# Kernel optimization log

Measured on AMD Instinct MI355X. Metric: run time of the kernel, lower is better.

Reference implementation:

```python
import jax, jax.numpy as jnp
from jax import lax
import numpy as np

SCALES = 3
DIR_PROFILE = [2, 3, 4]


def _gaussian_lowpass():
    ks, sigma = 5, 1.0
    ax = np.arange(-ks // 2 + 1.0, ks // 2 + 1.0)
    g = np.exp(-0.5 * np.square(ax) / sigma ** 2)
    k1 = g / g.sum()
    k2 = np.outer(k1, k1)
    k2 = k2 / k2.sum()
    return k2.astype(np.float32)  # [5, 5]


def _oriented_filter(angle, scale):
    size = 15
    sx, sy = 2.0 * scale, 0.5 * scale
    x = np.arange(-size // 2 + 1, size // 2 + 1)
    y = np.arange(-size // 2 + 1, size // 2 + 1)
    X, Y = np.meshgrid(x, y)
    Xr = X * np.cos(angle) - Y * np.sin(angle)
    Yr = X * np.sin(angle) + Y * np.cos(angle)
    k = np.exp(-0.5 * (Xr ** 2 / sx ** 2 + Yr ** 2 / sy ** 2)) * Xr / sx ** 2
    k = k - k.mean()
    n = np.linalg.norm(k)
    if n > 1e-6:
        k = k / n
    return k.astype(np.float32)  # [15, 15]


LP_FILTER = jnp.asarray(_gaussian_lowpass())[None, None]  # [1,1,5,5]
DIR_FILTERS = []  # per scale: [n_dirs, 1, 15, 15]
for _s, _lvl in enumerate(DIR_PROFILE):
    _nd = 2 ** _lvl
    _fs = np.stack([_oriented_filter(np.pi * d / _nd, _s + 1) for d in range(_nd)])
    DIR_FILTERS.append(jnp.asarray(_fs)[:, None])


def _depthwise(x, kernel):
    # x: [N, 1, H, W]; kernel: [O, 1, kh, kw]; reflect-pad 'same' cross-correlation
    kh, kw = kernel.shape[2], kernel.shape[3]
    xp = jnp.pad(x, ((0, 0), (0, 0), (kh // 2, kh // 2), (kw // 2, kw // 2)), mode='reflect')
    return lax.conv_general_dilated(xp, kernel, (1, 1), 'VALID',
                                    dimension_numbers=('NCHW', 'OIHW', 'NCHW'))


def setup_inputs() -> dict:
    key = jax.random.key(0)
    x = jax.random.normal(key, (8, 3, 384, 384), dtype=jnp.float32)
    return {"x": x}


def reference(x) -> jnp.ndarray:
    B, C, H, W = x.shape
    xc = x.reshape(B * C, 1, H, W)  # each RGB channel processed independently

    # Non-subsampled Laplacian pyramid: bandpasses + final lowpass
    bandpasses = []
    current = xc
    for _ in range(SCALES):
        lp = _depthwise(current, LP_FILTER)
        bandpasses.append(current - lp)
        current = lp

    # Directional filter bank per scale (all directions in one grouped conv)
    feats = []
    for s in range(SCALES):
        feats.append(_depthwise(bandpasses[s], DIR_FILTERS[s]))  # [B*C, 2^lvl, H, W]
    feats.append(current)  # final lowpass [B*C, 1, H, W]

    out = jnp.concatenate(feats, axis=1)  # [B*C, 29, H, W]
    return out.reshape(B, C * out.shape[1], H, W)  # [B, 87, H, W]
```

## Files before the change

kernel.cpp:

```cpp
#include <hip/hip_runtime.h>

#define HH 384
#define WW 384
#define HWSZ (HH * WW)
#define NIMG 24

#define SYM0 0
#define ASYM0 126
#define SYM1 238
#define ASYM1 490
#define SYM2 714
#define ASYM2 1218

__device__ __forceinline__ int refl(int i, int n) {
    if (i < 0) i = -i;
    if (i >= n) i = 2 * n - 2 - i;
    return i;
}

__device__ const float LPW[5] = {
    0.054488684549642945f, 0.24420134200323332f, 0.40261994689424746f,
    0.24420134200323332f, 0.054488684549642945f
};

__global__ __launch_bounds__(256) void gen_filters(double* __restrict__ gtmp) {
    int f = blockIdx.x;
    int s, d, nd;
    if (f < 4)       { s = 0; nd = 4;  d = f;      }
    else if (f < 12) { s = 1; nd = 8;  d = f - 4;  }
    else             { s = 2; nd = 16; d = f - 12; }

    double angle = M_PI * (double)d / (double)nd;
    double scale = (double)(s + 1);
    double sx = 2.0 * scale, sy = 0.5 * scale;

    int tid = threadIdx.x;
    double val = 0.0;
    if (tid < 225) {
        int row = tid / 15, col = tid % 15;
        double X = (double)(col - 7);
        double Y = (double)(row - 7);
        double ca = cos(angle), sa = sin(angle);
        double Xr = X * ca - Y * sa;
        double Yr = X * sa + Y * ca;
        val = exp(-0.5 * (Xr * Xr / (sx * sx) + Yr * Yr / (sy * sy))) * Xr / (sx * sx);
    }

    __shared__ double red[256];
    red[tid] = val;
    __syncthreads();
    for (int st = 128; st > 0; st >>= 1) {
        if (tid < st) red[tid] += red[tid + st];
        __syncthreads();
    }
    double mean = red[0] / 225.0;
    __syncthreads();

    double dv = (tid < 225) ? (val - mean) : 0.0;
    red[tid] = dv * dv;
    __syncthreads();
    for (int st = 128; st > 0; st >>= 1) {
        if (tid < st) red[tid] += red[tid + st];
        __syncthreads();
    }
    double nrm = sqrt(red[0]);
    double inv = (nrm > 1e-6) ? (1.0 / nrm) : 1.0;

    if (tid < 225) {
        gtmp[(long)f * 225 + tid] = (val - mean) * inv;
    }
}

__global__ __launch_bounds__(256) void pack_tables(
    const double* __restrict__ gtmp, float* __restrict__ tab) {
    int s = blockIdx.x;
    int nh = (s == 0) ? 2 : (s == 1) ? 4 : 8;
    int fbase = (s == 0) ? 0 : (s == 1) ? 4 : 12;
    int symoff = (s == 0) ? SYM0 : (s == 1) ? SYM1 : SYM2;
    int asymoff = (s == 0) ? ASYM0 : (s == 1) ? ASYM1 : ASYM2;
    int nsym = 63 * nh, nasym = 56 * nh;

    for (int t = threadIdx.x; t < nsym + nasym; t += 256) {
        bool issym = t < nsym;
        int tt = issym ? t : t - nsym;
        int j = tt / nh, k = tt % nh;
        int u, v;
        if (issym) {
            if (j < 7)       { u = 0;         v = j + 1; }
            else if (j < 14) { u = j - 6;     v = 0;     }
            else { int p = j - 14; u = p / 7 + 1; v = p % 7 + 1; }
        } else {
            if (j < 7)       { u = 0;         v = j + 1; }
            else { int p = j - 7; u = p / 7 + 1; v = p % 7 + 1; }
        }
        int d = (k == 0) ? (issym ? nh : 0) : k;
        const double* F = gtmp + (long)(fbase + d) * 225;
        double gp = F[(7 + u) * 15 + (7 + v)];
        double gm = F[(7 + u) * 15 + (7 - v)];
        double val = issym ? 0.5 * (gp + gm) : 0.5 * (gp - gm);
        tab[(issym ? symoff : asymoff) + j * nh + k] = (float)val;
    }
}

__global__ __launch_bounds__(256) void lp_kernel(
    const float* __restrict__ in, float* __restrict__ out, long ostride) {
    int n = blockIdx.z;
    int x = blockIdx.x * 32 + threadIdx.x;
    int y = blockIdx.y * 8 + threadIdx.y;
    const float* ip = in + (long)n * HWSZ;

    float acc = 0.f;
#pragma unroll
    for (int fy = 0; fy < 5; ++fy) {
        int yy = refl(y + fy - 2, HH);
        const float* rp = ip + yy * WW;
        float rs = 0.f;
#pragma unroll
        for (int fx = 0; fx < 5; ++fx) {
            int xx = refl(x + fx - 2, WW);
            rs = fmaf(LPW[fx], rp[xx], rs);
        }
        acc = fmaf(LPW[fy], rs, acc);
    }
    out[(long)n * ostride + y * WW + x] = acc;
}

template <int NH, int R>
__global__ __launch_bounds__(256, 4) void dir_kernel(
    const float* __restrict__ A, long as,
    const float* __restrict__ B, long bs,
    const float* __restrict__ symt, const float* __restrict__ asymt,
    float* __restrict__ out, int c0) {
    constexpr int TH = 8 * R;
    __shared__ float sm[TH + 14][48];

    int n = blockIdx.z;
    int tx = threadIdx.x, ty = threadIdx.y;
    int bx = blockIdx.x * 32, by = blockIdx.y * TH;

    const float* Ab = A + (long)n * as;
    const float* Bb = B + (long)n * bs;

    int lid = ty * 32 + tx;
    for (int l = lid; l < (TH + 14) * 46; l += 256) {
        int ly = l / 46, lx = l % 46;
        int gy = refl(by + ly - 7, HH);
        int gx = refl(bx + lx - 7, WW);
        long gi = (long)gy * WW + gx;
        sm[ly][lx] = Ab[gi] - Bb[gi];
    }
    __syncthreads();

    float accP[NH][R], accQ[NH][R];
#pragma unroll
    for (int k = 0; k < NH; ++k)
#pragma unroll
        for (int r = 0; r < R; ++r) { accP[k][r] = 0.f; accQ[k][r] = 0.f; }

    int xc = tx + 7;

#pragma unroll
    for (int v = 1; v <= 7; ++v) {
        float dv[R];
#pragma unroll
        for (int r = 0; r < R; ++r) {
            int yb = ty + 7 + 8 * r;
            dv[r] = sm[yb][xc + v] - sm[yb][xc - v];
        }
#pragma unroll
        for (int k = 0; k < NH; ++k) {
            float cs = symt[(v - 1) * NH + k];
            float ca = asymt[(v - 1) * NH + k];
#pragma unroll
            for (int r = 0; r < R; ++r) {
                accP[k][r] = fmaf(cs, dv[r], accP[k][r]);
                accQ[k][r] = fmaf(ca, dv[r], accQ[k][r]);
            }
        }
    }

#pragma unroll 1
    for (int u = 1; u <= 7; ++u) {
        {
            float dvc[R];
#pragma unroll
            for (int r = 0; r < R; ++r) {
                int yb = ty + 7 + 8 * r;
                dvc[r] = sm[yb + u][xc] - sm[yb - u][xc];
            }
#pragma unroll
            for (int k = 0; k < NH; ++k) {
                float cs = symt[(6 + u) * NH + k];
#pragma unroll
                for (int r = 0; r < R; ++r)
                    accP[k][r] = fmaf(cs, dvc[r], accP[k][r]);
            }
        }
#pragma unroll
        for (int v = 1; v <= 7; ++v) {
            float S[R], D[R];
#pragma unroll
            for (int r = 0; r < R; ++r) {
                int yb = ty + 7 + 8 * r;
                float a = sm[yb + u][xc + v];
                float b = sm[yb + u][xc - v];
                float c = sm[yb - u][xc + v];
                float d = sm[yb - u][xc - v];
                float t1 = a - d, t2 = b - c;
                S[r] = t1 + t2;
                D[r] = t1 - t2;
            }
            int jp = (u - 1) * 7 + (v - 1);
#pragma unroll
            for (int k = 0; k < NH; ++k) {
                float cs = symt[(14 + jp) * NH + k];
                float ca = asymt[(7 + jp) * NH + k];
#pragma unroll
                for (int r = 0; r < R; ++r) {
                    accP[k][r] = fmaf(cs, S[r], accP[k][r]);
                    accQ[k][r] = fmaf(ca, D[r], accQ[k][r]);
                }
            }
        }
    }

    long ob = ((long)n * 29 + c0) * HWSZ;
#pragma unroll
    for (int r = 0; r < R; ++r) {
        long idx = ob + (long)(by + ty + r * 8) * WW + bx + tx;
        out[idx] = accQ[0][r];
        out[idx + (long)NH * HWSZ] = accP[0][r];
#pragma unroll
        for (int k = 1; k < NH; ++k) {
            out[idx + (long)k * HWSZ] = accP[k][r] + accQ[k][r];
            out[idx + (long)(2 * NH - k) * HWSZ] = accP[k][r] - accQ[k][r];
        }
    }
}

extern "C" void kernel_launch(void* const* d_in, const int* in_sizes, int n_in,
                              void* d_out, int out_size, void* d_ws, size_t ws_size,
                              hipStream_t stream) {
    const float* x = (const float*)d_in[0];
    float* out = (float*)d_out;
    float* ws = (float*)d_ws;

    float* tab = ws;
    float* lp0 = ws + 2048;
    float* lp1 = lp0 + (long)NIMG * HWSZ;
    double* gtmp = (double*)lp0;

    gen_filters<<<28, 256, 0, stream>>>(gtmp);
    pack_tables<<<3, 256, 0, stream>>>(gtmp, tab);

    dim3 blk(32, 8);
    dim3 lpgrid(12, 48, NIMG);
    lp_kernel<<<lpgrid, blk, 0, stream>>>(x, lp0, HWSZ);
    lp_kernel<<<lpgrid, blk, 0, stream>>>(lp0, lp1, HWSZ);
    lp_kernel<<<lpgrid, blk, 0, stream>>>(lp1, out + 28l * HWSZ, 29l * HWSZ);

    dir_kernel<2, 4><<<dim3(12, 12, NIMG), blk, 0, stream>>>(
        x, HWSZ, lp0, HWSZ, tab + SYM0, tab + ASYM0, out, 0);
    dir_kernel<4, 4><<<dim3(12, 12, NIMG), blk, 0, stream>>>(
        lp0, HWSZ, lp1, HWSZ, tab + SYM1, tab + ASYM1, out, 4);
    dir_kernel<8, 2><<<dim3(12, 24, NIMG), blk, 0, stream>>>(
        lp1, HWSZ, out + 28l * HWSZ, 29l * HWSZ, tab + SYM2, tab + ASYM2, out, 12);
}
```

Before: 638.4 us.

## Fuse lowpass pyramid into one kernel and bake filter tables at compile time

The three separate lowpass launches become one tiled kernel that loads a haloed input tile into shared memory and runs the separable 5-tap filter three times in place, writing lp0, lp1 and the final lowpass. The two filter-generation and table-packing kernels are replaced by constexpr tables evaluated at compile time, so coefficients become immediates in the fully unrolled directional loop. The unrolled loop may raise register pressure or code size. The fused lowpass also recomputes halo rows and adds several block barriers.

```diff
diff --git a/kernel.cpp b/kernel.cpp
--- a/kernel.cpp
+++ b/kernel.cpp
@@ -5,13 +5,6 @@
 #define HWSZ (HH * WW)
 #define NIMG 24
 
-#define SYM0 0
-#define ASYM0 126
-#define SYM1 238
-#define ASYM1 490
-#define SYM2 714
-#define ASYM2 1218
-
 __device__ __forceinline__ int refl(int i, int n) {
     if (i < 0) i = -i;
     if (i >= n) i = 2 * n - 2 - i;
@@ -23,113 +16,206 @@
     0.24420134200323332f, 0.054488684549642945f
 };
 
-__global__ __launch_bounds__(256) void gen_filters(double* __restrict__ gtmp) {
-    int f = blockIdx.x;
-    int s, d, nd;
-    if (f < 4)       { s = 0; nd = 4;  d = f;      }
-    else if (f < 12) { s = 1; nd = 8;  d = f - 4;  }
-    else             { s = 2; nd = 16; d = f - 12; }
-
-    double angle = M_PI * (double)d / (double)nd;
+constexpr double CPI = 3.141592653589793;
+
+constexpr double cexp(double x) {
+    int k = 0; double t = x;
+    while (t > 0.25 || t < -0.25) { t *= 0.5; ++k; }
+    double sum = 1.0, term = 1.0;
+    for (int n = 1; n <= 14; ++n) { term *= t / n; sum += term; }
+    for (int i = 0; i < k; ++i) sum *= sum;
+    return sum;
+}
+constexpr double ccos(double x) {
+    double sgn = 1.0;
+    if (x > CPI * 0.5) { x = CPI - x; sgn = -1.0; }
+    double x2 = x * x, sum = 1.0, term = 1.0;
+    for (int n = 1; n <= 12; ++n) { term *= -x2 / ((2.0 * n - 1) * (2.0 * n)); sum += term; }
+    return sgn * sum;
+}
+constexpr double csin(double x) {
+    if (x > CPI * 0.5) x = CPI - x;
+    double x2 = x * x, sum = x, term = x;
+    for (int n = 1; n <= 12; ++n) { term *= -x2 / ((2.0 * n) * (2.0 * n + 1)); sum += term; }
+    return sum;
+}
+constexpr double csqrt(double x) {
+    if (x <= 0.0) return 0.0;
+    double y = x > 1.0 ? x : 1.0;
+    for (int i = 0; i < 80; ++i) y = 0.5 * (y + x / y);
+    return y;
+}
+
+struct F225 { double v[225]; };
+
+constexpr F225 make_filter(int s, int d, int nd) {
+    double angle = CPI * (double)d / (double)nd;
     double scale = (double)(s + 1);
     double sx = 2.0 * scale, sy = 0.5 * scale;
-
-    int tid = threadIdx.x;
-    double val = 0.0;
-    if (tid < 225) {
-        int row = tid / 15, col = tid % 15;
-        double X = (double)(col - 7);
-        double Y = (double)(row - 7);
-        double ca = cos(angle), sa = sin(angle);
-        double Xr = X * ca - Y * sa;
-        double Yr = X * sa + Y * ca;
-        val = exp(-0.5 * (Xr * Xr / (sx * sx) + Yr * Yr / (sy * sy))) * Xr / (sx * sx);
-    }
-
-    __shared__ double red[256];
-    red[tid] = val;
-    __syncthreads();
-    for (int st = 128; st > 0; st >>= 1) {
-        if (tid < st) red[tid] += red[tid + st];
-        __syncthreads();
-    }
-    double mean = red[0] / 225.0;
-    __syncthreads();
-
-    double dv = (tid < 225) ? (val - mean) : 0.0;
-    red[tid] = dv * dv;
-    __syncthreads();
-    for (int st = 128; st > 0; st >>= 1) {
-        if (tid < st) red[tid] += red[tid + st];
-        __syncthreads();
-    }
-    double nrm = sqrt(red[0]);
-    double inv = (nrm > 1e-6) ? (1.0 / nrm) : 1.0;
-
-    if (tid < 225) {
-        gtmp[(long)f * 225 + tid] = (val - mean) * inv;
-    }
-}
-
-__global__ __launch_bounds__(256) void pack_tables(
-    const double* __restrict__ gtmp, float* __restrict__ tab) {
-    int s = blockIdx.x;
-    int nh = (s == 0) ? 2 : (s == 1) ? 4 : 8;
-    int fbase = (s == 0) ? 0 : (s == 1) ? 4 : 12;
-    int symoff = (s == 0) ? SYM0 : (s == 1) ? SYM1 : SYM2;
-    int asymoff = (s == 0) ? ASYM0 : (s == 1) ? ASYM1 : ASYM2;
-    int nsym = 63 * nh, nasym = 56 * nh;
-
-    for (int t = threadIdx.x; t < nsym + nasym; t += 256) {
-        bool issym = t < nsym;
-        int tt = issym ? t : t - nsym;
-        int j = tt / nh, k = tt % nh;
+    double ca = ccos(angle), sa = csin(angle);
+    F225 f{};
+    double sum = 0.0;
+    for (int r = 0; r < 15; ++r)
+        for (int c = 0; c < 15; ++c) {
+            double X = (double)(c - 7), Y = (double)(r - 7);
+            double Xr = X * ca - Y * sa;
+            double Yr = X * sa + Y * ca;
+            double k = cexp(-0.5 * (Xr * Xr / (sx * sx) + Yr * Yr / (sy * sy))) * Xr / (sx * sx);
+            f.v[r * 15 + c] = k; sum += k;
+        }
+    double mean = sum / 225.0;
+    double ss = 0.0;
+    for (int i = 0; i < 225; ++i) { f.v[i] -= mean; ss += f.v[i] * f.v[i]; }
+    double n = csqrt(ss);
+    if (n > 1e-6) for (int i = 0; i < 225; ++i) f.v[i] /= n;
+    return f;
+}
+
+template <int S, int D>
+struct Filt { static constexpr F225 v = make_filter(S, D, S == 0 ? 4 : (S == 1 ? 8 : 16)); };
+
+constexpr const F225& getF(int s, int d) {
+    if (s == 0) {
+        if (d == 0) return Filt<0, 0>::v;
+        if (d == 1) return Filt<0, 1>::v;
+        return Filt<0, 2>::v;
+    } else if (s == 1) {
+        if (d == 0) return Filt<1, 0>::v;
+        if (d == 1) return Filt<1, 1>::v;
+        if (d == 2) return Filt<1, 2>::v;
+        if (d == 3) return Filt<1, 3>::v;
+        return Filt<1, 4>::v;
+    } else {
+        if (d == 0) return Filt<2, 0>::v;
+        if (d == 1) return Filt<2, 1>::v;
+        if (d == 2) return Filt<2, 2>::v;
+        if (d == 3) return Filt<2, 3>::v;
+        if (d == 4) return Filt<2, 4>::v;
+        if (d == 5) return Filt<2, 5>::v;
+        if (d == 6) return Filt<2, 6>::v;
+        if (d == 7) return Filt<2, 7>::v;
+        return Filt<2, 8>::v;
+    }
+}
+
+template <int NH> struct PTab { float a[63 * NH]; float b[63 * NH]; };
+
+template <int NH>
+constexpr PTab<NH> make_ptab(int s) {
+    PTab<NH> t{};
+    for (int j = 0; j < 63; ++j) {
         int u, v;
-        if (issym) {
-            if (j < 7)       { u = 0;         v = j + 1; }
-            else if (j < 14) { u = j - 6;     v = 0;     }
-            else { int p = j - 14; u = p / 7 + 1; v = p % 7 + 1; }
-        } else {
-            if (j < 7)       { u = 0;         v = j + 1; }
-            else { int p = j - 7; u = p / 7 + 1; v = p % 7 + 1; }
-        }
-        int d = (k == 0) ? (issym ? nh : 0) : k;
-        const double* F = gtmp + (long)(fbase + d) * 225;
-        double gp = F[(7 + u) * 15 + (7 + v)];
-        double gm = F[(7 + u) * 15 + (7 - v)];
-        double val = issym ? 0.5 * (gp + gm) : 0.5 * (gp - gm);
-        tab[(issym ? symoff : asymoff) + j * nh + k] = (float)val;
-    }
-}
-
-__global__ __launch_bounds__(256) void lp_kernel(
-    const float* __restrict__ in, float* __restrict__ out, long ostride) {
+        if (j < 7)       { u = 0;     v = j + 1; }
+        else if (j < 14) { u = j - 6; v = 0;     }
+        else { int p = j - 14; u = p / 7 + 1; v = p % 7 + 1; }
+        for (int k = 0; k < NH; ++k) {
+            int dP = (k == 0) ? NH : k;
+            int dQ = (k == 0) ? 0 : k;
+            const F225& FP = getF(s, dP);
+            const F225& FQ = getF(s, dQ);
+            double A = 0.5 * (FP.v[(7 + u) * 15 + (7 + v)] + FP.v[(7 + u) * 15 + (7 - v)]);
+            double B = 0.5 * (FQ.v[(7 + u) * 15 + (7 + v)] - FQ.v[(7 + u) * 15 + (7 - v)]);
+            t.a[j * NH + k] = (float)A;
+            t.b[j * NH + k] = (float)B;
+        }
+    }
+    return t;
+}
+template <int S, int NH>
+struct PTbl { static constexpr PTab<NH> t = make_ptab<NH>(S); };
+
+__global__ __launch_bounds__(256, 4) void lp_fused(
+    const float* __restrict__ in, float* __restrict__ lp0g,
+    float* __restrict__ lp1g, float* __restrict__ outall) {
+    __shared__ float sIN[44][48];
+    __shared__ float sA[44][40];
+    __shared__ float sB[40][40];
+
     int n = blockIdx.z;
-    int x = blockIdx.x * 32 + threadIdx.x;
-    int y = blockIdx.y * 8 + threadIdx.y;
+    int bx = blockIdx.x * 32, by = blockIdx.y * 32;
+    int tid = threadIdx.y * 32 + threadIdx.x;
+    int yy = threadIdx.y, xx = threadIdx.x;
     const float* ip = in + (long)n * HWSZ;
 
-    float acc = 0.f;
-#pragma unroll
-    for (int fy = 0; fy < 5; ++fy) {
-        int yy = refl(y + fy - 2, HH);
-        const float* rp = ip + yy * WW;
-        float rs = 0.f;
-#pragma unroll
-        for (int fx = 0; fx < 5; ++fx) {
-            int xx = refl(x + fx - 2, WW);
-            rs = fmaf(LPW[fx], rp[xx], rs);
-        }
-        acc = fmaf(LPW[fy], rs, acc);
-    }
-    out[(long)n * ostride + y * WW + x] = acc;
-}
-
-template <int NH, int R>
+    for (int l = tid; l < 44 * 44; l += 256) {
+        int r = l / 44, c = l % 44;
+        sIN[r][c] = ip[(long)refl(by + r - 6, HH) * WW + refl(bx + c - 6, WW)];
+    }
+    __syncthreads();
+    for (int l = tid; l < 44 * 40; l += 256) {
+        int r = l / 40, c = l % 40;
+        float s = 0.f;
+#pragma unroll
+        for (int i = 0; i < 5; ++i) s = fmaf(LPW[i], sIN[r][c + i], s);
+        sA[r][c] = s;
+    }
+    __syncthreads();
+    for (int l = tid; l < 40 * 40; l += 256) {
+        int r = l / 40, c = l % 40;
+        float s = 0.f;
+#pragma unroll
+        for (int i = 0; i < 5; ++i) s = fmaf(LPW[i], sA[r + i][c], s);
+        sB[r][c] = s;
+    }
+    __syncthreads();
+    {
+        float* l0 = lp0g + (long)n * HWSZ;
+#pragma unroll
+        for (int rr = 0; rr < 4; ++rr)
+            l0[(long)(by + yy + rr * 8) * WW + bx + xx] = sB[yy + rr * 8 + 4][xx + 4];
+        float* h1 = &sIN[0][0];
+        for (int l = tid; l < 40 * 36; l += 256) {
+            int r = l / 36, c = l % 36;
+            float s = 0.f;
+#pragma unroll
+            for (int i = 0; i < 5; ++i) s = fmaf(LPW[i], sB[r][c + i], s);
+            h1[r * 36 + c] = s;
+        }
+    }
+    __syncthreads();
+    {
+        const float* h1 = &sIN[0][0];
+        for (int l = tid; l < 36 * 36; l += 256) {
+            int r = l / 36, c = l % 36;
+            float s = 0.f;
+#pragma unroll
+            for (int i = 0; i < 5; ++i) s = fmaf(LPW[i], h1[(r + i) * 36 + c], s);
+            sB[r][c] = s;
+        }
+    }
+    __syncthreads();
+    {
+        float* l1 = lp1g + (long)n * HWSZ;
+#pragma unroll
+        for (int rr = 0; rr < 4; ++rr)
+            l1[(long)(by + yy + rr * 8) * WW + bx + xx] = sB[yy + rr * 8 + 2][xx + 2];
+        float* h2 = &sA[0][0];
+        for (int l = tid; l < 36 * 32; l += 256) {
+            int r = l / 32, c = l % 32;
+            float s = 0.f;
+#pragma unroll
+            for (int i = 0; i < 5; ++i) s = fmaf(LPW[i], sB[r][c + i], s);
+            h2[r * 32 + c] = s;
+        }
+    }
+    __syncthreads();
+    {
+        const float* h2 = &sA[0][0];
+#pragma unroll
+        for (int rr = 0; rr < 4; ++rr) {
+            int r = yy + rr * 8;
+            float s = 0.f;
+#pragma unroll
+            for (int i = 0; i < 5; ++i) s = fmaf(LPW[i], h2[(r + i) * 32 + xx], s);
+            outall[((long)n * 29 + 28) * HWSZ + (long)(by + r) * WW + bx + xx] = s;
+        }
+    }
+}
+
+template <int SIDX, int NH, int R>
 __global__ __launch_bounds__(256, 4) void dir_kernel(
     const float* __restrict__ A, long as,
     const float* __restrict__ B, long bs,
-    const float* __restrict__ symt, const float* __restrict__ asymt,
     float* __restrict__ out, int c0) {
     constexpr int TH = 8 * R;
     __shared__ float sm[TH + 14][48];
@@ -169,17 +255,14 @@
         }
 #pragma unroll
         for (int k = 0; k < NH; ++k) {
-            float cs = symt[(v - 1) * NH + k];
-            float ca = asymt[(v - 1) * NH + k];
-#pragma unroll
-            for (int r = 0; r < R; ++r) {
-                accP[k][r] = fmaf(cs, dv[r], accP[k][r]);
+            float ca = PTbl<SIDX, NH>::t.b[(v - 1) * NH + k];
+#pragma unroll
+            for (int r = 0; r < R; ++r)
                 accQ[k][r] = fmaf(ca, dv[r], accQ[k][r]);
-            }
-        }
-    }
-
-#pragma unroll 1
+        }
+    }
+
+#pragma unroll
     for (int u = 1; u <= 7; ++u) {
         {
             float dvc[R];
@@ -190,7 +273,7 @@
             }
 #pragma unroll
             for (int k = 0; k < NH; ++k) {
-                float cs = symt[(6 + u) * NH + k];
+                float cs = PTbl<SIDX, NH>::t.a[(6 + u) * NH + k];
 #pragma unroll
                 for (int r = 0; r < R; ++r)
                     accP[k][r] = fmaf(cs, dvc[r], accP[k][r]);
@@ -210,11 +293,11 @@
                 S[r] = t1 + t2;
                 D[r] = t1 - t2;
             }
-            int jp = (u - 1) * 7 + (v - 1);
+            int jp = 14 + (u - 1) * 7 + (v - 1);
 #pragma unroll
             for (int k = 0; k < NH; ++k) {
-                float cs = symt[(14 + jp) * NH + k];
-                float ca = asymt[(7 + jp) * NH + k];
+                float cs = PTbl<SIDX, NH>::t.a[jp * NH + k];
+                float ca = PTbl<SIDX, NH>::t.b[jp * NH + k];
 #pragma unroll
                 for (int r = 0; r < R; ++r) {
                     accP[k][r] = fmaf(cs, S[r], accP[k][r]);
@@ -245,24 +328,16 @@
     float* out = (float*)d_out;
     float* ws = (float*)d_ws;
 
-    float* tab = ws;
-    float* lp0 = ws + 2048;
+    float* lp0 = ws;
     float* lp1 = lp0 + (long)NIMG * HWSZ;
-    double* gtmp = (double*)lp0;
-
-    gen_filters<<<28, 256, 0, stream>>>(gtmp);
-    pack_tables<<<3, 256, 0, stream>>>(gtmp, tab);
 
     dim3 blk(32, 8);
-    dim3 lpgrid(12, 48, NIMG);
-    lp_kernel<<<lpgrid, blk, 0, stream>>>(x, lp0, HWSZ);
-    lp_kernel<<<lpgrid, blk, 0, stream>>>(lp0, lp1, HWSZ);
-    lp_kernel<<<lpgrid, blk, 0, stream>>>(lp1, out + 28l * HWSZ, 29l * HWSZ);
-
-    dir_kernel<2, 4><<<dim3(12, 12, NIMG), blk, 0, stream>>>(
-        x, HWSZ, lp0, HWSZ, tab + SYM0, tab + ASYM0, out, 0);
-    dir_kernel<4, 4><<<dim3(12, 12, NIMG), blk, 0, stream>>>(
-        lp0, HWSZ, lp1, HWSZ, tab + SYM1, tab + ASYM1, out, 4);
-    dir_kernel<8, 2><<<dim3(12, 24, NIMG), blk, 0, stream>>>(
-        lp1, HWSZ, out + 28l * HWSZ, 29l * HWSZ, tab + SYM2, tab + ASYM2, out, 12);
-}
+    lp_fused<<<dim3(12, 12, NIMG), blk, 0, stream>>>(x, lp0, lp1, out);
+
+    dir_kernel<0, 2, 4><<<dim3(12, 12, NIMG), blk, 0, stream>>>(
+        x, HWSZ, lp0, HWSZ, out, 0);
+    dir_kernel<1, 4, 4><<<dim3(12, 12, NIMG), blk, 0, stream>>>(
+        lp0, HWSZ, lp1, HWSZ, out, 4);
+    dir_kernel<2, 8, 2><<<dim3(12, 24, NIMG), blk, 0, stream>>>(
+        lp1, HWSZ, out + 28l * HWSZ, 29l * HWSZ, out, 12);
+}
```

Result: slower. 1.066 ms (+67.0%).
